# Optimization experiments

Hardware: AMD Instinct MI355X
Metric: run time of the kernel (lower is better)

The kernel has to match this reference:

```python
import jax, jax.numpy as jnp
import numpy as np

B, S, D = 16, 2048, 128


def setup_inputs() -> dict:
    key = jax.random.key(0)
    kq, kk, kv = jax.random.split(key, 3)
    return {
        "queries": jax.random.normal(kq, (B, S, D), dtype=jnp.float32),
        "keys": jax.random.normal(kk, (B, S, D), dtype=jnp.float32),
        "values": jax.random.normal(kv, (B, S, D), dtype=jnp.float32),
        "mask": jnp.zeros((B, S, S), dtype=bool),  # True -> masked out
    }


def reference(queries, keys, values, mask):
    d_k = queries.shape[-1]
    scale = 1.0 / np.sqrt(d_k).astype(np.float32)
    # scores: [B, S, S]
    scores = jnp.einsum("bqd,bkd->bqk", queries, keys) * scale
    scores = jnp.where(mask, -jnp.inf, scores)
    attn_weights = jax.nn.softmax(scores, axis=-1)
    # dropout prob = 0.0 (eval), identity
    output = jnp.einsum("bqk,bkd->bqd", attn_weights, values)
    return output
```

## Files before the change

kernel.cpp:

```cpp
#include <hip/hip_runtime.h>
#include <hip/hip_bf16.h>

#define SEQ    2048
#define DIM    128
#define NBATCH 16
#define KVB    32
#define NSPLIT 2
#define HALFS  (SEQ / NSPLIT)
#define NTILE  (HALFS / KVB)
#define QW     16
#define NWAVE  4
#define QB     (QW * NWAVE)
#define NROW   (NBATCH * SEQ)
#define TELEM  (KVB * DIM)

typedef __bf16 bf16x8 __attribute__((ext_vector_type(8)));
typedef float  f32x4  __attribute__((ext_vector_type(4)));
typedef unsigned int uint;

#define LOG2E  1.44269504088896340736f
#define NEGINF (-__builtin_inff())

#define CVT_PK(d, lo, hi) asm("v_cvt_pk_bf16_f32 %0, %1, %2" : "=v"(d) : "v"(lo), "v"(hi))
#define SWAP32(x, y) asm("v_permlane32_swap_b32 %0, %1" : "+v"(x), "+v"(y))
#define SWAP16(x, y) asm("v_permlane16_swap_b32 %0, %1" : "+v"(x), "+v"(y))

typedef const __attribute__((address_space(1))) uint* gup;
typedef       __attribute__((address_space(3))) uint* lup;
#define GLDS16(g, l) __builtin_amdgcn_global_load_lds((gup)(g), (lup)(l), 16, 0, 0)

#define APPLY_MASK(mw, s)                          \
    if (mw) {                                      \
        if (mw & 0x000000ffu) s[0] = NEGINF;       \
        if (mw & 0x0000ff00u) s[1] = NEGINF;       \
        if (mw & 0x00ff0000u) s[2] = NEGINF;       \
        if (mw & 0xff000000u) s[3] = NEGINF;       \
    }

__global__ __launch_bounds__(256)
void sdpa_prep(const float* __restrict__ Kg, const float* __restrict__ Vg,
               __bf16* __restrict__ Kb, __bf16* __restrict__ Vb)
{
    const int tile = (int)blockIdx.x;
    const int tid  = (int)threadIdx.x;
    const size_t row0 = (size_t)tile * KVB;

    {
        const int kr = tid >> 3;
        const int c2 = (tid & 7) * 2;
        const int kx = kr & 7;
        const float* src = Kg + (row0 + kr) * DIM;
        __bf16* dst = Kb + (size_t)tile * TELEM + (size_t)kr * DIM;
        #pragma unroll
        for (int c = 0; c < 2; ++c) {
            const int ci = c2 + c;
            const int sc = ci ^ kx;
            const float4 a = *(const float4*)(src + sc * 8);
            const float4 b = *(const float4*)(src + sc * 8 + 4);
            bf16x8 h;
            h[0]=(__bf16)a.x; h[1]=(__bf16)a.y; h[2]=(__bf16)a.z; h[3]=(__bf16)a.w;
            h[4]=(__bf16)b.x; h[5]=(__bf16)b.y; h[6]=(__bf16)b.z; h[7]=(__bf16)b.w;
            *(bf16x8*)(dst + ci * 8) = h;
        }
    }
    {
        const int vd = tid & 127;
        const int cp = (tid >> 7) * 2;
        const int vx = (vd >> 1) & 3;
        const float* src = Vg + row0 * DIM + vd;
        __bf16* dst = Vb + (size_t)tile * TELEM + (size_t)vd * KVB;
        #pragma unroll
        for (int c = 0; c < 2; ++c) {
            const int ck = cp + c;
            const int ci = ck ^ vx;
            bf16x8 h;
            #pragma unroll
            for (int j = 0; j < 8; ++j) h[j] = (__bf16)src[(size_t)(ck * 8 + j) * DIM];
            *(bf16x8*)(dst + ci * 8) = h;
        }
    }
}

__global__ __launch_bounds__(256, 4)
void sdpa_main(const float* __restrict__ Qg, const __bf16* __restrict__ Kbf,
               const __bf16* __restrict__ Vbf, const unsigned char* __restrict__ Mg,
               float* __restrict__ Uw, float* __restrict__ Lw)
{
    __shared__ __bf16 Ksh[2][TELEM];
    __shared__ __bf16 Vsh[2][TELEM];

    const int tid  = (int)threadIdx.x;
    const int wid  = tid >> 6;
    const int lane = tid & 63;
    const int lg   = lane >> 4;
    const int lr   = lane & 15;

    const int bid  = (int)blockIdx.x;
    const int nbid = (bid & 7) * 128 + (bid >> 3);
    const int half = nbid & 1;
    const int qt   = nbid >> 1;
    const int bb   = qt >> 5;
    const int qtl  = qt & 31;
    const int q0w  = qtl * QB + wid * QW;

    const float qscale = 0.08838834764831845f * LOG2E;

    bf16x8 aq[4];
    {
        const float* qrow = Qg + ((size_t)(bb * SEQ + q0w + lr)) * DIM;
        #pragma unroll
        for (int kb = 0; kb < 4; ++kb) {
            const float4 f0 = *(const float4*)(qrow + kb * 32 + lg * 8);
            const float4 f1 = *(const float4*)(qrow + kb * 32 + lg * 8 + 4);
            bf16x8 h;
            h[0] = (__bf16)(f0.x * qscale); h[1] = (__bf16)(f0.y * qscale);
            h[2] = (__bf16)(f0.z * qscale); h[3] = (__bf16)(f0.w * qscale);
            h[4] = (__bf16)(f1.x * qscale); h[5] = (__bf16)(f1.y * qscale);
            h[6] = (__bf16)(f1.z * qscale); h[7] = (__bf16)(f1.w * qscale);
            aq[kb] = h;
        }
    }

    const __bf16* Kt0 = Kbf + (size_t)(bb * 64 + half * 32) * TELEM;
    const __bf16* Vt0 = Vbf + (size_t)(bb * 64 + half * 32) * TELEM;
    const unsigned char* Mrow = Mg + (size_t)bb * SEQ * SEQ
                              + (size_t)(q0w + lr) * SEQ + half * HALFS;

    uint mn0, mn1;
    const int loff = lane * 16;

    auto issue = [&](int t, int b) {
        const char* Ks = (const char*)(Kt0 + (size_t)t * TELEM);
        const char* Vs = (const char*)(Vt0 + (size_t)t * TELEM);
        char* Kd = (char*)Ksh[b];
        char* Vd = (char*)Vsh[b];
        #pragma unroll
        for (int j = 0; j < 2; ++j) {
            const int o = wid * 1024 + j * 4096;
            GLDS16(Ks + o + loff, Kd + o);
            GLDS16(Vs + o + loff, Vd + o);
        }
        const unsigned char* ms = Mrow + t * KVB + lg * 4;
        mn0 = *(const uint*)(ms);
        mn1 = *(const uint*)(ms + 16);
    };

    issue(0, 0);

    f32x4 acc[8];
    #pragma unroll
    for (int i = 0; i < 8; ++i) acc[i] = (f32x4)(0.0f);
    float l_run = 0.0f;

    const int kxr = lr & 7;
    const int vxr = (lr >> 1) & 3;

    for (int t = 0; t < NTILE; ++t) {
        asm volatile("s_waitcnt vmcnt(0)" ::: "memory");
        __syncthreads();
        const uint mw0 = mn0, mw1 = mn1;
        if (t + 1 < NTILE) issue(t + 1, (t + 1) & 1);

        const bf16x8* const Kc = (const bf16x8*)Ksh[t & 1];
        const bf16x8* const Vc = (const bf16x8*)Vsh[t & 1];

        f32x4 s0 = (f32x4)(0.0f), s1 = (f32x4)(0.0f);
        __builtin_amdgcn_s_setprio(1);
        #pragma unroll
        for (int kb = 0; kb < 4; ++kb) {
            const int ch = (kb * 4 + lg) ^ kxr;
            const bf16x8 a0 = Kc[(lr)      * 16 + ch];
            const bf16x8 a1 = Kc[(16 + lr) * 16 + ch];
            s0 = __builtin_amdgcn_mfma_f32_16x16x32_bf16(a0, aq[kb], s0, 0, 0, 0);
            s1 = __builtin_amdgcn_mfma_f32_16x16x32_bf16(a1, aq[kb], s1, 0, 0, 0);
        }
        __builtin_amdgcn_s_setprio(0);

        APPLY_MASK(mw0, s0) APPLY_MASK(mw1, s1)

        float ps = 0.0f;
        #pragma unroll
        for (int r = 0; r < 4; ++r) { s0[r] = __builtin_amdgcn_exp2f(s0[r]); ps += s0[r]; }
        #pragma unroll
        for (int r = 0; r < 4; ++r) { s1[r] = __builtin_amdgcn_exp2f(s1[r]); ps += s1[r]; }
        l_run += ps;

        bf16x8 ap;
        {
            uint a0w, a1w, b0w, b1w;
            CVT_PK(a0w, s0[0], s0[1]); CVT_PK(a1w, s0[2], s0[3]);
            CVT_PK(b0w, s1[0], s1[1]); CVT_PK(b1w, s1[2], s1[3]);
            SWAP32(a0w, b0w); SWAP16(a0w, b0w);
            SWAP32(a1w, b1w); SWAP16(a1w, b1w);
            union W { uint w[4]; bf16x8 v; } u;
            u.w[0] = a0w; u.w[1] = a1w; u.w[2] = b0w; u.w[3] = b1w;
            ap = u.v;
        }

        __builtin_amdgcn_s_setprio(1);
        #pragma unroll
        for (int nt = 0; nt < 8; ++nt) {
            const bf16x8 bv = Vc[(nt * 16 + lr) * 4 + (lg ^ vxr)];
            acc[nt] = __builtin_amdgcn_mfma_f32_16x16x32_bf16(ap, bv, acc[nt], 0, 0, 0);
        }
        __builtin_amdgcn_s_setprio(0);
    }

    l_run += __shfl_xor(l_run, 16);
    l_run += __shfl_xor(l_run, 32);
    if (lg == 0)
        Lw[(size_t)half * NROW + bb * SEQ + q0w + lr] = l_run;

    float* ub = Uw + ((size_t)half * NROW + bb * SEQ + q0w + lg * 4) * DIM + lr;
    #pragma unroll
    for (int r = 0; r < 4; ++r)
        #pragma unroll
        for (int nt = 0; nt < 8; ++nt)
            ub[(size_t)r * DIM + nt * 16] = acc[nt][r];
}

__global__ __launch_bounds__(256)
void sdpa_combine(float* __restrict__ Og, const float* __restrict__ Uw,
                  const float* __restrict__ Lw)
{
    const int gid = (int)blockIdx.x * 256 + (int)threadIdx.x;
    const int row = gid >> 5;
    const float inv = 1.0f / (Lw[row] + Lw[NROW + row]);
    const float4* U0 = (const float4*)Uw;
    const float4* U1 = (const float4*)(Uw + (size_t)NROW * DIM);
    const float4 a = U0[gid];
    const float4 b = U1[gid];
    float4 o;
    o.x = (a.x + b.x) * inv; o.y = (a.y + b.y) * inv;
    o.z = (a.z + b.z) * inv; o.w = (a.w + b.w) * inv;
    ((float4*)Og)[gid] = o;
}

extern "C" void kernel_launch(void* const* d_in, const int* in_sizes, int n_in,
                              void* d_out, int out_size, void* d_ws, size_t ws_size,
                              hipStream_t stream) {
    const float* Q = (const float*)d_in[0];
    const float* K = (const float*)d_in[1];
    const float* V = (const float*)d_in[2];
    const unsigned char* M = (const unsigned char*)d_in[3];
    float* O  = (float*)d_out;
    float*  Uw  = (float*)d_ws;
    float*  Lw  = Uw + (size_t)NSPLIT * NROW * DIM;
    __bf16* Kbf = (__bf16*)(Lw + (size_t)NSPLIT * NROW);
    __bf16* Vbf = Kbf + (size_t)NROW * DIM;
    sdpa_prep<<<dim3(NROW / KVB), dim3(256), 0, stream>>>(K, V, Kbf, Vbf);
    sdpa_main<<<dim3(NBATCH * 32 * NSPLIT), dim3(256), 0, stream>>>(Q, Kbf, Vbf, M, Uw, Lw);
    sdpa_combine<<<dim3(NROW * DIM / 4 / 256), dim3(256), 0, stream>>>(O, Uw, Lw);
}
```

Measured before the change: 77.64 us.

## Drop KV split and combine kernel; use 2-wave blocks over full sequence

Removes the two-way split of the key/value sequence and the separate combine kernel. Each block now holds 2 waves (32 query rows) and walks all 64 KV tiles, normalizing by the row sum and writing the output directly. This avoids writing and re-reading the partial-output workspace and saves a kernel launch. In exchange each block runs a serial loop twice as long, and the smaller blocks share each staged K/V tile across fewer waves, so LDS staging is amortized over less compute.

```diff
diff --git a/kernel.cpp b/kernel.cpp
--- a/kernel.cpp
+++ b/kernel.cpp
@@ -5,11 +5,9 @@
 #define DIM    128
 #define NBATCH 16
 #define KVB    32
-#define NSPLIT 2
-#define HALFS  (SEQ / NSPLIT)
-#define NTILE  (HALFS / KVB)
+#define NTILE  (SEQ / KVB)
 #define QW     16
-#define NWAVE  4
+#define NWAVE  2
 #define QB     (QW * NWAVE)
 #define NROW   (NBATCH * SEQ)
 #define TELEM  (KVB * DIM)
@@ -81,10 +79,10 @@
     }
 }
 
-__global__ __launch_bounds__(256, 4)
+__global__ __launch_bounds__(128, 4)
 void sdpa_main(const float* __restrict__ Qg, const __bf16* __restrict__ Kbf,
                const __bf16* __restrict__ Vbf, const unsigned char* __restrict__ Mg,
-               float* __restrict__ Uw, float* __restrict__ Lw)
+               float* __restrict__ Og)
 {
     __shared__ __bf16 Ksh[2][TELEM];
     __shared__ __bf16 Vsh[2][TELEM];
@@ -97,10 +95,8 @@
 
     const int bid  = (int)blockIdx.x;
     const int nbid = (bid & 7) * 128 + (bid >> 3);
-    const int half = nbid & 1;
-    const int qt   = nbid >> 1;
-    const int bb   = qt >> 5;
-    const int qtl  = qt & 31;
+    const int bb   = nbid >> 6;
+    const int qtl  = nbid & 63;
     const int q0w  = qtl * QB + wid * QW;
 
     const float qscale = 0.08838834764831845f * LOG2E;
@@ -121,10 +117,10 @@
         }
     }
 
-    const __bf16* Kt0 = Kbf + (size_t)(bb * 64 + half * 32) * TELEM;
-    const __bf16* Vt0 = Vbf + (size_t)(bb * 64 + half * 32) * TELEM;
+    const __bf16* Kt0 = Kbf + (size_t)(bb * 64) * TELEM;
+    const __bf16* Vt0 = Vbf + (size_t)(bb * 64) * TELEM;
     const unsigned char* Mrow = Mg + (size_t)bb * SEQ * SEQ
-                              + (size_t)(q0w + lr) * SEQ + half * HALFS;
+                              + (size_t)(q0w + lr) * SEQ;
 
     uint mn0, mn1;
     const int loff = lane * 16;
@@ -135,8 +131,8 @@
         char* Kd = (char*)Ksh[b];
         char* Vd = (char*)Vsh[b];
         #pragma unroll
-        for (int j = 0; j < 2; ++j) {
-            const int o = wid * 1024 + j * 4096;
+        for (int j = 0; j < 4; ++j) {
+            const int o = wid * 1024 + j * 2048;
             GLDS16(Ks + o + loff, Kd + o);
             GLDS16(Vs + o + loff, Vd + o);
         }
@@ -208,32 +204,19 @@
 
     l_run += __shfl_xor(l_run, 16);
     l_run += __shfl_xor(l_run, 32);
-    if (lg == 0)
-        Lw[(size_t)half * NROW + bb * SEQ + q0w + lr] = l_run;
-
-    float* ub = Uw + ((size_t)half * NROW + bb * SEQ + q0w + lg * 4) * DIM + lr;
+
+    float inv[4];
+    #pragma unroll
+    for (int r = 0; r < 4; ++r) {
+        const float lq = __shfl(l_run, (lane & 48) | (lg * 4 + r));
+        inv[r] = 1.0f / lq;
+    }
+    float* orow = Og + ((size_t)(bb * SEQ + q0w + lg * 4)) * DIM + lr;
     #pragma unroll
     for (int r = 0; r < 4; ++r)
         #pragma unroll
         for (int nt = 0; nt < 8; ++nt)
-            ub[(size_t)r * DIM + nt * 16] = acc[nt][r];
-}
-
-__global__ __launch_bounds__(256)
-void sdpa_combine(float* __restrict__ Og, const float* __restrict__ Uw,
-                  const float* __restrict__ Lw)
-{
-    const int gid = (int)blockIdx.x * 256 + (int)threadIdx.x;
-    const int row = gid >> 5;
-    const float inv = 1.0f / (Lw[row] + Lw[NROW + row]);
-    const float4* U0 = (const float4*)Uw;
-    const float4* U1 = (const float4*)(Uw + (size_t)NROW * DIM);
-    const float4 a = U0[gid];
-    const float4 b = U1[gid];
-    float4 o;
-    o.x = (a.x + b.x) * inv; o.y = (a.y + b.y) * inv;
-    o.z = (a.z + b.z) * inv; o.w = (a.w + b.w) * inv;
-    ((float4*)Og)[gid] = o;
+            orow[(size_t)r * DIM + nt * 16] = acc[nt][r] * inv[r];
 }
 
 extern "C" void kernel_launch(void* const* d_in, const int* in_sizes, int n_in,
@@ -244,11 +227,8 @@
     const float* V = (const float*)d_in[2];
     const unsigned char* M = (const unsigned char*)d_in[3];
     float* O  = (float*)d_out;
-    float*  Uw  = (float*)d_ws;
-    float*  Lw  = Uw + (size_t)NSPLIT * NROW * DIM;
-    __bf16* Kbf = (__bf16*)(Lw + (size_t)NSPLIT * NROW);
+    __bf16* Kbf = (__bf16*)d_ws;
     __bf16* Vbf = Kbf + (size_t)NROW * DIM;
     sdpa_prep<<<dim3(NROW / KVB), dim3(256), 0, stream>>>(K, V, Kbf, Vbf);
-    sdpa_main<<<dim3(NBATCH * 32 * NSPLIT), dim3(256), 0, stream>>>(Q, Kbf, Vbf, M, Uw, Lw);
-    sdpa_combine<<<dim3(NROW * DIM / 4 / 256), dim3(256), 0, stream>>>(O, Uw, Lw);
+    sdpa_main<<<dim3(NROW / QB), dim3(128), 0, stream>>>(Q, Kbf, Vbf, M, O);
 }
```

Measured after the change: 83.71 us. +7.8%, slower.
